# Kernel tuning notes

Measured on AMD Instinct MI355X. Metric: run time of the kernel, lower is better.

Reference implementation:

```python
import jax, jax.numpy as jnp
import numpy as np

SPANS = [15, 9, 5]   # processed largest-first, matching sorted(span_groups, reverse=True)
DEPTH = 2
TOL = 1.5


def _rmsnorm(x, eps=1e-5):
    return x * jax.lax.rsqrt(jnp.mean(x * x, axis=-1, keepdims=True) + eps)


def _block(m, g, Wi, Wz, Wdt, bdt, alog, Wo, Wyg):
    """Dual-input gated selective-scan block (stand-in for create_multihead_block
    block_type='dual_input'): match stream runs a diagonal SSM scan over window
    tokens, gated by the geometry stream; both streams are residually updated."""
    u = _rmsnorm(m) @ Wi                              # [P,L,C]
    z = jax.nn.silu(_rmsnorm(g) @ Wz)                 # [P,L,C] geom gate
    delta = jax.nn.softplus(u @ Wdt + bdt)            # [P,L,C]
    decay = jnp.exp(delta * (-jnp.exp(alog)))         # [P,L,C]
    x_in = delta * u

    def step(h, inp):
        d, xi = inp
        h = d * h + xi
        return h, h

    _, hs = jax.lax.scan(step, jnp.zeros_like(x_in[:, 0]),
                         (jnp.swapaxes(decay, 0, 1), jnp.swapaxes(x_in, 0, 1)))
    y = jnp.swapaxes(hs, 0, 1) * z                    # [P,L,C]
    return m + y @ Wo, g + jax.nn.silu(y @ Wyg)


def _sample(feat_flat, ys, xs, H, W):
    """Bilinear sampling, align_corners=True, padding_mode='zeros'.
    feat_flat: [C, H*W]; ys, xs: [L] float coords. Returns [L, C]."""
    y0 = jnp.floor(ys); x0 = jnp.floor(xs)
    wy = ys - y0; wx = xs - x0

    def tap(yi, xi):
        valid = ((yi >= 0) & (yi <= H - 1) & (xi >= 0) & (xi <= W - 1)).astype(feat_flat.dtype)
        idx = (jnp.clip(yi, 0, H - 1).astype(jnp.int32) * W
               + jnp.clip(xi, 0, W - 1).astype(jnp.int32))
        return feat_flat[:, idx] * valid              # [C,L]

    v = (tap(y0, x0) * (1 - wy) * (1 - wx) + tap(y0, x0 + 1) * (1 - wy) * wx
         + tap(y0 + 1, x0) * wy * (1 - wx) + tap(y0 + 1, x0 + 1) * wy * wx)
    return v.T


def _process_side(feat_m, feat_g, flow, sx, sy, params):
    B, C, H, W = feat_m.shape
    G = feat_g.shape[1]
    Wi, Wz, Wdt, bdt, alog, Wo, Wyg = params
    dt = feat_m.dtype
    bb, yy, xx = [a.ravel() for a in jnp.meshgrid(jnp.arange(B), jnp.arange(H), jnp.arange(W), indexing='ij')]
    # flow-shifted sub-pixel window centers, clamped (flow[...,0]=dx, flow[...,1]=dy)
    cy = jnp.clip(yy.astype(dt) + flow[bb, yy, xx, 1], 0, H - 1)
    cx = jnp.clip(xx.astype(dt) + flow[bb, yy, xx, 0], 0, W - 1)
    avg = ((sx + sy) * 0.5).ravel()
    assigned = jnp.zeros(avg.shape, dtype=bool)
    fm = feat_m.reshape(B, C, H * W)
    fg = feat_g.reshape(B, G, H * W)
    out_m = jnp.zeros((B * H * W, C), dt)
    out_g = jnp.zeros((B * H * W, G), dt)
    wsum = jnp.zeros((B * H * W,), dt)
    for si, s in enumerate(SPANS):
        # span-group mask; positions claimed by a larger span are excluded
        mask = (jnp.abs(avg - s) < TOL) & (~assigned)
        assigned = assigned | mask
        h = s // 2
        dy, dx = [a.ravel() for a in jnp.meshgrid(jnp.arange(-h, h + 1), jnp.arange(-h, h + 1), indexing='ij')]
        dist = jnp.sqrt((dy * dy + dx * dx).astype(dt))
        pw = jnp.exp(-dist / (s / 2.0))
        pw = pw / pw.sum()                             # normalized distance weights [L]
        ys = cy[:, None] + dy[None, :].astype(dt)      # [P,L]
        xs = cx[:, None] + dx[None, :].astype(dt)
        wm = jax.vmap(lambda b, y, x: _sample(fm[b], y, x, H, W))(bb, ys, xs)  # [P,L,C]
        wg = jax.vmap(lambda b, y, x: _sample(fg[b], y, x, H, W))(bb, ys, xs)  # [P,L,G]
        for d in range(DEPTH):
            wm, wg = _block(wm, wg, Wi[si, d], Wz[si, d], Wdt[si, d], bdt[si, d], alog[si, d], Wo[si, d], Wyg[si, d])
        # scatter-accumulate around the integer center position
        ty = yy[:, None] + dy[None, :]
        tx = xx[:, None] + dx[None, :]
        valid = ((ty >= 0) & (ty < H) & (tx >= 0) & (tx < W)).astype(dt)
        w = pw[None, :] * mask[:, None].astype(dt) * valid           # [P,L]
        idx = bb[:, None] * (H * W) + jnp.clip(ty, 0, H - 1) * W + jnp.clip(tx, 0, W - 1)
        out_m = out_m.at[idx.ravel()].add((wm * w[..., None]).reshape(-1, C))
        out_g = out_g.at[idx.ravel()].add((wg * w[..., None]).reshape(-1, G))
        wsum = wsum.at[idx.ravel()].add(w.ravel())
    ws = jnp.maximum(wsum, 1e-6)[:, None]
    om = (out_m / ws).reshape(B, H, W, C).transpose(0, 3, 1, 2)
    og = (out_g / ws).reshape(B, H, W, G).transpose(0, 3, 1, 2)
    return om, og


def setup_inputs() -> dict:
    key = jax.random.key(0)
    ks = jax.random.split(key, 18)
    B, C, G, H, W = 1, 128, 64, 28, 28
    f32 = jnp.float32
    d = {}
    d['feat_match_0'] = jax.random.normal(ks[0], (B, C, H, W), f32)
    d['feat_match_1'] = jax.random.normal(ks[1], (B, C, H, W), f32)
    d['feat_geom_0'] = jax.random.normal(ks[2], (B, G, H, W), f32)
    d['feat_geom_1'] = jax.random.normal(ks[3], (B, G, H, W), f32)
    d['flow_map_0'] = 1.5 * jax.random.normal(ks[4], (B, H, W, 4), f32)
    d['flow_map_1'] = 1.5 * jax.random.normal(ks[5], (B, H, W, 4), f32)
    # spans in [3, 17) so each span group {5, 9, 15} is populated
    d['adaptive_spans_x_0'] = 3.0 + 14.0 * jax.random.uniform(ks[6], (B, H, W), f32)
    d['adaptive_spans_y_0'] = 3.0 + 14.0 * jax.random.uniform(ks[7], (B, H, W), f32)
    d['adaptive_spans_x_1'] = 3.0 + 14.0 * jax.random.uniform(ks[8], (B, H, W), f32)
    d['adaptive_spans_y_1'] = 3.0 + 14.0 * jax.random.uniform(ks[9], (B, H, W), f32)
    # per-span (order [15,9,5]) x per-depth block parameters
    d['W_in'] = jax.random.normal(ks[10], (3, DEPTH, C, C), f32) / np.sqrt(C).astype(np.float32)
    d['W_z'] = jax.random.normal(ks[11], (3, DEPTH, G, C), f32) / np.sqrt(G).astype(np.float32)
    d['W_dt'] = jax.random.normal(ks[12], (3, DEPTH, C, C), f32) / np.sqrt(C).astype(np.float32)
    d['b_dt'] = 0.1 * jax.random.normal(ks[13], (3, DEPTH, C), f32)
    d['a_log'] = 0.1 * jax.random.normal(ks[14], (3, DEPTH, C), f32)
    d['W_out'] = jax.random.normal(ks[15], (3, DEPTH, C, C), f32) / np.sqrt(C).astype(np.float32)
    d['W_yg'] = jax.random.normal(ks[16], (3, DEPTH, C, G), f32) / np.sqrt(C).astype(np.float32)
    return d


def reference(feat_match_0, feat_match_1, feat_geom_0, feat_geom_1,
              flow_map_0, flow_map_1,
              adaptive_spans_x_0, adaptive_spans_y_0,
              adaptive_spans_x_1, adaptive_spans_y_1,
              W_in, W_z, W_dt, b_dt, a_log, W_out, W_yg):
    params = (W_in, W_z, W_dt, b_dt, a_log, W_out, W_yg)
    m0, g0 = _process_side(feat_match_0, feat_geom_0, flow_map_0[..., :2],
                           adaptive_spans_x_0, adaptive_spans_y_0, params)
    m1, g1 = _process_side(feat_match_1, feat_geom_1, flow_map_1[..., :2],
                           adaptive_spans_x_1, adaptive_spans_y_1, params)
    return m0, m1, g0, g1
```

## Files before the change

### kernel.cpp

```cpp
#include <hip/hip_runtime.h>
#include <math.h>

typedef short s16x8 __attribute__((ext_vector_type(8)));
typedef unsigned short u16x8v __attribute__((ext_vector_type(8)));
typedef float f32x4 __attribute__((ext_vector_type(4)));
typedef _Float16 h2 __attribute__((ext_vector_type(2)));

#define HH 28
#define WW 28
#define PP 784
#define CC 128
#define GG 64
#define MT 48
#define NH 3
#define AST 136
#define GSTB 72

#define OFF_FMT0 0
#define OFF_FMT1 100352
#define OFF_FGT0 200704
#define OFF_FGT1 250880
#define OFF_ACCM0 301056
#define OFF_ACCM1 401408
#define OFF_ACCG0 501760
#define OFF_ACCG1 551936
#define OFF_ACCW0 602112
#define OFF_ACCW1 602896
#define ACC_FLOATS 302624
#define OFF_CNT   603680
#define OFF_CNT2  603704
#define OFF_JOB   603728
#define OFF_WB    605296

#define WIB 0
#define WZB 98304
#define WDB 147456
#define WOB 245760
#define WYB 344064

struct KArgs {
  const float* fm[2]; const float* fg[2];
  const float* flow[2]; const float* sx[2]; const float* sy[2];
  const float* Wi; const float* Wz; const float* Wdt; const float* bdt;
  const float* alog; const float* Wo; const float* Wyg;
  float* fmT[2]; float* fgT[2];
  float* accm[2]; float* accg[2]; float* accw[2];
  int* cnt; int* cnt2; int* job;
  unsigned short* wb;
  float* out;
};

__device__ __forceinline__ int span_group(float avg, int& s) {
  if (fabsf(avg - 15.f) < 1.5f) { s = 15; return 0; }
  if (fabsf(avg - 9.f)  < 1.5f) { s = 9;  return 1; }
  if (fabsf(avg - 5.f)  < 1.5f) { s = 5;  return 2; }
  s = 0; return 3;
}

__device__ __forceinline__ float fast_silu(float x) {
  return x * __builtin_amdgcn_rcpf(1.f + __expf(-x));
}

__device__ __forceinline__ unsigned short f2bf(float f) {
  unsigned u = __float_as_uint(f);
  unsigned r = (u + 0x7fffu + ((u >> 16) & 1u)) >> 16;
  return (unsigned short)r;
}
__device__ __forceinline__ float b2f(unsigned short u) {
  return __uint_as_float(((unsigned)u) << 16);
}

__device__ __forceinline__ void atomic_pk2(_Float16* base, float x, float y) {
  h2 v; v[0] = (_Float16)x; v[1] = (_Float16)y;
#if __has_builtin(__builtin_amdgcn_global_atomic_fadd_v2f16)
  __builtin_amdgcn_global_atomic_fadd_v2f16((h2*)base, v);
#else
  unsigned* a = (unsigned*)base;
  unsigned old = *a, assumed;
  do {
    assumed = old;
    h2 cur = *(h2*)&assumed;
    h2 nw; nw[0] = cur[0] + v[0]; nw[1] = cur[1] + v[1];
    old = atomicCAS(a, assumed, *(unsigned*)&nw);
  } while (old != assumed);
#endif
}

#define MFMA(A_, B_, C_) __builtin_amdgcn_mfma_f32_16x16x32_bf16((A_), (B_), (C_), 0, 0, 0)

__global__ void k_zero(float* p, int n) {
  int j = blockIdx.x * 256 + threadIdx.x;
  if (j < n) p[j] = 0.f;
}

__global__ void k_prep(KArgs a) {
  int j = blockIdx.x * 256 + threadIdx.x;
  int side = j / 150528; int r = j - side * 150528;
  int p = r / 192; int ch = r - p * 192;
  if (ch < CC) a.fmT[side][p * CC + ch] = a.fm[side][ch * PP + p];
  else         a.fgT[side][p * GG + (ch - CC)] = a.fg[side][(ch - CC) * PP + p];
}

__global__ void k_prepw(KArgs a) {
  int j = blockIdx.x * 256 + threadIdx.x;
  unsigned short* wb = a.wb;
  if (j < 98304) {
    int set = j >> 14, r = j & 16383; int o = r >> 7, c = r & 127;
    wb[WIB + j] = f2bf(a.Wi[set * 16384 + c * 128 + o]);
  } else if (j < 147456) {
    int r = j - 98304; int set = r >> 13, rr = r & 8191; int o = rr >> 6, c = rr & 63;
    wb[WZB + r] = f2bf(a.Wz[set * 8192 + c * 128 + o]);
  } else if (j < 245760) {
  } else if (j < 344064) {
    int r = j - 245760; int set = r >> 14, rr = r & 16383; int o = rr >> 7, c = rr & 127;
    wb[WOB + r] = f2bf(a.Wo[set * 16384 + c * 128 + o]);
  } else {
    int r = j - 344064; int set = r >> 13, rr = r & 8191; int o = rr >> 7, c = rr & 127;
    wb[WYB + r] = f2bf(a.Wyg[set * 8192 + c * 64 + o]);
  }
}

__global__ void k_prepwid(KArgs a) {
  __shared__ float wi_row[128];
  const int set = blockIdx.x, i = blockIdx.y, o = threadIdx.x;
  wi_row[o] = a.Wi[set * 16384 + i * 128 + o];
  __syncthreads();
  float acc = 0.f;
#pragma unroll 4
  for (int m = 0; m < 128; ++m) acc = fmaf(wi_row[m], a.Wdt[set * 16384 + m * 128 + o], acc);
  a.wb[WDB + set * 16384 + o * 128 + i] = f2bf(acc);
}

__global__ void k_count(KArgs a) {
  int j = blockIdx.x * 256 + threadIdx.x;
  if (j >= 2 * PP) return;
  a.job[j] = -1;
  int side = j / PP, p = j - side * PP;
  float avg = 0.5f * (a.sx[side][p] + a.sy[side][p]);
  int s; int g = span_group(avg, s);
  if (g < 3) {
    int py = p / WW, px = p - py * WW;
    int region = (py / 14) * 4 + px / 7;
    atomicAdd(&a.cnt[region * 3 + g], 1);
  }
}

__global__ void k_assign(KArgs a) {
  int j = blockIdx.x * 256 + threadIdx.x;
  if (j >= 2 * PP) return;
  int side = j / PP, p = j - side * PP;
  float avg = 0.5f * (a.sx[side][p] + a.sy[side][p]);
  int s; int g = span_group(avg, s);
  if (g < 3) {
    int py = p / WW, px = p - py * WW;
    int region = (py / 14) * 4 + px / 7;
    int base = 0;
    for (int gg = 0; gg < g; ++gg) base += a.cnt[region * 3 + gg];
    int rank = base + atomicAdd(&a.cnt2[region * 3 + g], 1);
    a.job[region + 8 * rank] = (side << 10) | p;
  }
}

__global__ void k_fin(KArgs a) {
  int j = blockIdx.x * 256 + threadIdx.x;
  int side = j / 150528; int r = j - side * 150528;
  int p = r / 192; int ch = r - p * 192;
  float inv = 1.f / fmaxf(a.accw[side][p], 1e-6f);
  if (ch < CC) {
    const _Float16* amh = (const _Float16*)a.accm[side];
    a.out[side * 100352 + ch * PP + p] = (float)amh[p * CC + ch] * inv;
  } else {
    const _Float16* agh = (const _Float16*)a.accg[side];
    a.out[200704 + side * 50176 + (ch - CC) * PP + p] = (float)agh[p * GG + (ch - CC)] * inv;
  }
}

__launch_bounds__(256, 2)
__global__ void k_main(KArgs a) {
  __shared__ __align__(16) unsigned short mres[2][MT * AST];
  __shared__ __align__(16) unsigned short gres[2][MT * GSTB];
  __shared__ __align__(16) unsigned short bufA[MT * AST];
  __shared__ __align__(16) unsigned short bufB[MT * GSTB];
  __shared__ float hs[2 * CC];
  __shared__ float na_s[2 * CC];
  __shared__ float bb_s[2 * CC];
  __shared__ float pw_l[228];
  __shared__ int   tap_i[MT * 4];
  __shared__ float tap_w[MT * 4];
  __shared__ int   sc_i[2][MT];
  __shared__ float sc_w[2][MT];
  __shared__ float red[4];

  const int tid = threadIdx.x;
  const int job = a.job[blockIdx.x];
  if (job < 0) return;
  const int side = job >> 10, p = job & 1023;
  const float avg = 0.5f * (a.sx[side][p] + a.sy[side][p]);
  int s; const int si = span_group(avg, s);
  const int hspan = s >> 1, L = s * s;
  const int py = p / WW, px = p - py * WW;
  const float fdx = a.flow[side][p * 4 + 0], fdy = a.flow[side][p * 4 + 1];
  const float cy = fminf(fmaxf((float)py + fdy, 0.f), (float)(HH - 1));
  const float cx = fminf(fmaxf((float)px + fdx, 0.f), (float)(WW - 1));
  const float* fmT = a.fmT[side]; const float* fgT = a.fgT[side];
  _Float16* accm_h = (_Float16*)a.accm[side];
  _Float16* accg_h = (_Float16*)a.accg[side];
  float* accw = a.accw[side];

  const unsigned short* wb = a.wb;
  const int wv = tid >> 6, l = tid & 63, lm = l & 15, g = l >> 4;
  const int o0 = 32 * wv + lm, o1 = o0 + 16, og = 16 * wv + lm;
  const int ttk = tid >> 3, c8 = tid & 7;

  { const int d2 = tid >> 7, c2 = tid & 127;
    na_s[tid] = -__expf(a.alog[(si * 2 + d2) * CC + c2]);
    bb_s[tid] = a.bdt[(si * 2 + d2) * CC + c2];
    hs[tid] = 0.f; }
  if (tid < L) {
    const int dyi = tid / s - hspan, dxi = tid % s - hspan;
    pw_l[tid] = __expf(-sqrtf((float)(dyi * dyi + dxi * dxi)) / (0.5f * (float)s));
  }
  __syncthreads();
  { float v = (tid < L) ? pw_l[tid] : 0.f;
#pragma unroll
    for (int off = 32; off > 0; off >>= 1) v += __shfl_xor(v, off);
    if ((tid & 63) == 0) red[tid >> 6] = v; }
  __syncthreads();
  { const float pinv = 1.f / (red[0] + red[1] + red[2] + red[3]);
    if (tid < L) pw_l[tid] *= pinv; }
  __syncthreads();

  auto comp_taps = [&](int t0_, int b_) {
    if (tid < MT) {
      const int t = t0_ + tid;
      if (t < L) {
        const int tq = t / s;
        const int dyi = tq - hspan, dxi = (t - tq * s) - hspan;
        const float ys = cy + (float)dyi, xs = cx + (float)dxi;
        const float y0f = floorf(ys), x0f = floorf(xs);
        const float wy = ys - y0f, wx = xs - x0f;
        const int y0 = (int)y0f, x0 = (int)x0f;
#pragma unroll
        for (int k = 0; k < 4; ++k) {
          const int yi = y0 + (k >> 1), xi = x0 + (k & 1);
          const bool v = (yi >= 0) && (yi < HH) && (xi >= 0) && (xi < WW);
          const int yc = min(max(yi, 0), HH - 1), xc = min(max(xi, 0), WW - 1);
          tap_i[tid * 4 + k] = yc * WW + xc;
          const float wgt = ((k >> 1) ? wy : 1.f - wy) * ((k & 1) ? wx : 1.f - wx);
          tap_w[tid * 4 + k] = v ? wgt : 0.f;
        }
        const int ty = py + dyi, tx = px + dxi;
        const bool sv = (ty >= 0) && (ty < HH) && (tx >= 0) && (tx < WW);
        const int sid2 = sv ? ty * WW + tx : 0;
        const float sw = sv ? pw_l[t] : 0.f;
        sc_i[b_][tid] = sid2; sc_w[b_][tid] = sw;
        if (sw != 0.f) atomicAdd(&accw[sid2], sw);
      } else {
#pragma unroll
        for (int k = 0; k < 4; ++k) { tap_i[tid * 4 + k] = 0; tap_w[tid * 4 + k] = 0.f; }
        sc_i[b_][tid] = 0; sc_w[b_][tid] = 0.f;
      }
    }
  };

  auto sample_tile = [&](int b_) {
    for (int tk = ttk; tk < MT; tk += 32) {
      const int* ti = &tap_i[tk * 4]; const float* tw = &tap_w[tk * 4];
      f32x4 am0 = {0.f,0.f,0.f,0.f}, am1 = am0, am2 = am0, am3 = am0;
      f32x4 ag0 = am0, ag1 = am0;
#pragma unroll
      for (int k2 = 0; k2 < 4; ++k2) {
        const float w = tw[k2];
        const float* pm = &fmT[ti[k2] * CC + c8 * 16];
        am0 += w * *(const f32x4*)&pm[0];
        am1 += w * *(const f32x4*)&pm[4];
        am2 += w * *(const f32x4*)&pm[8];
        am3 += w * *(const f32x4*)&pm[12];
        const float* pg = &fgT[ti[k2] * GG + c8 * 8];
        ag0 += w * *(const f32x4*)&pg[0];
        ag1 += w * *(const f32x4*)&pg[4];
      }
      u16x8v w0, w1, wg;
#pragma unroll
      for (int j = 0; j < 4; ++j) {
        w0[j] = f2bf(am0[j]); w0[4 + j] = f2bf(am1[j]);
        w1[j] = f2bf(am2[j]); w1[4 + j] = f2bf(am3[j]);
        wg[j] = f2bf(ag0[j]); wg[4 + j] = f2bf(ag1[j]);
      }
      *(u16x8v*)&mres[b_][tk * AST + c8 * 16] = w0;
      *(u16x8v*)&mres[b_][tk * AST + c8 * 16 + 8] = w1;
      *(u16x8v*)&gres[b_][tk * GSTB + c8 * 8] = wg;
    }
  };

  const int nt = (L + MT - 1) / MT;
  comp_taps(0, 0);
  __syncthreads();
  sample_tile(0);
  int cur = 0;

  for (int t = 0; t < nt; ++t) {
    const int t0 = t * MT;
    const int tlen = min(MT, L - t0);
    const int nxt = cur ^ 1;
    __syncthreads();
    if (t + 1 < nt) comp_taps(t0 + MT, nxt);

    for (int d = 0; d < 2; ++d) {
      const unsigned short* Wib  = wb + WIB + (si * 2 + d) * 16384;
      const unsigned short* Widb = wb + WDB + (si * 2 + d) * 16384;
      const unsigned short* Wzb  = wb + WZB + (si * 2 + d) * 8192;
      const unsigned short* Wob  = wb + WOB + (si * 2 + d) * 16384;
      const unsigned short* Wyb  = wb + WYB + (si * 2 + d) * 8192;
      if (d == 1) __syncthreads();
      for (int tk = ttk; tk < MT; tk += 32) {
        u16x8v m0 = *(const u16x8v*)&mres[cur][tk * AST + c8 * 16];
        u16x8v m1 = *(const u16x8v*)&mres[cur][tk * AST + c8 * 16 + 8];
        u16x8v gv = *(const u16x8v*)&gres[cur][tk * GSTB + c8 * 8];
        float mv[16], gvf[8];
#pragma unroll
        for (int k = 0; k < 8; ++k) { mv[k] = b2f(m0[k]); mv[8 + k] = b2f(m1[k]); gvf[k] = b2f(gv[k]); }
        float ssm = 0.f, ssg = 0.f;
#pragma unroll
        for (int k = 0; k < 16; ++k) ssm = fmaf(mv[k], mv[k], ssm);
#pragma unroll
        for (int k = 0; k < 8; ++k) ssg = fmaf(gvf[k], gvf[k], ssg);
#pragma unroll
        for (int off = 4; off > 0; off >>= 1) { ssm += __shfl_xor(ssm, off); ssg += __shfl_xor(ssg, off); }
        const float sm = rsqrtf(ssm * (1.f / CC) + 1e-5f);
        const float sgs = rsqrtf(ssg * (1.f / GG) + 1e-5f);
        u16x8v xa, xb, gx;
#pragma unroll
        for (int k = 0; k < 8; ++k) { xa[k] = f2bf(mv[k] * sm); xb[k] = f2bf(mv[8 + k] * sm); gx[k] = f2bf(gvf[k] * sgs); }
        *(u16x8v*)&bufA[tk * AST + c8 * 16] = xa;
        *(u16x8v*)&bufA[tk * AST + c8 * 16 + 8] = xb;
        *(u16x8v*)&bufB[tk * GSTB + c8 * 8] = gx;
      }
      __syncthreads();
      f32x4 u[NH][2], dt[NH][2], z[NH][2];
#pragma unroll
      for (int h = 0; h < NH; ++h)
#pragma unroll
        for (int j2 = 0; j2 < 2; ++j2) { u[h][j2] = (f32x4){0.f,0.f,0.f,0.f}; dt[h][j2] = (f32x4){0.f,0.f,0.f,0.f}; z[h][j2] = (f32x4){0.f,0.f,0.f,0.f}; }
#pragma unroll
      for (int ss = 0; ss < 4; ++ss) {
        const int c0 = 32 * ss + g * 8;
        const s16x8 bW0 = *(const s16x8*)&Wib[o0 * 128 + c0];
        const s16x8 bW1 = *(const s16x8*)&Wib[o1 * 128 + c0];
        const s16x8 bD0 = *(const s16x8*)&Widb[o0 * 128 + c0];
        const s16x8 bD1 = *(const s16x8*)&Widb[o1 * 128 + c0];
#pragma unroll
        for (int h = 0; h < NH; ++h) {
          s16x8 av = *(const s16x8*)&bufA[(h * 16 + lm) * AST + c0];
          u[h][0]  = MFMA(av, bW0, u[h][0]);
          u[h][1]  = MFMA(av, bW1, u[h][1]);
          dt[h][0] = MFMA(av, bD0, dt[h][0]);
          dt[h][1] = MFMA(av, bD1, dt[h][1]);
        }
      }
#pragma unroll
      for (int ss = 0; ss < 2; ++ss) {
        const int c0 = 32 * ss + g * 8;
        const s16x8 bZ0 = *(const s16x8*)&Wzb[o0 * 64 + c0];
        const s16x8 bZ1 = *(const s16x8*)&Wzb[o1 * 64 + c0];
#pragma unroll
        for (int h = 0; h < NH; ++h) {
          s16x8 gv2 = *(const s16x8*)&bufB[(h * 16 + lm) * GSTB + c0];
          z[h][0] = MFMA(gv2, bZ0, z[h][0]);
          z[h][1] = MFMA(gv2, bZ1, z[h][1]);
        }
      }
#pragma unroll
      for (int h = 0; h < NH; ++h)
#pragma unroll
        for (int j2 = 0; j2 < 2; ++j2)
#pragma unroll
          for (int r = 0; r < 4; ++r) z[h][j2][r] = fast_silu(z[h][j2][r]);

#pragma unroll
      for (int j2 = 0; j2 < 2; ++j2) {
        const int oc = j2 ? o1 : o0;
        const float bb = bb_s[d * CC + oc], na = na_s[d * CC + oc];
        float hcar = hs[d * CC + oc];
#pragma unroll
        for (int h = 0; h < NH; ++h) {
          float Pl[4], Dl[4]; float P = 0.f, D = 1.f;
#pragma unroll
          for (int r = 0; r < 4; ++r) {
            const float x = dt[h][j2][r] + bb;
            float dlt = fmaxf(x, 0.f) + __logf(1.f + __expf(-fabsf(x)));
            float dec = __expf(dlt * na), xin = dlt * u[h][j2][r];
            if (h * 16 + 4 * g + r >= tlen) { dec = 1.f; xin = 0.f; }
            P = dec * P + xin; D *= dec; Pl[r] = P; Dl[r] = D;
          }
          float Pi = P, Di = D;
          { float pa = __shfl_up(Pi, 16), da = __shfl_up(Di, 16);
            if (g >= 1) { Pi = Di * pa + Pi; Di *= da; }
            pa = __shfl_up(Pi, 32); da = __shfl_up(Di, 32);
            if (g >= 2) { Pi = Di * pa + Pi; Di *= da; } }
          float Pe = __shfl_up(Pi, 16), De = __shfl_up(Di, 16);
          if (g == 0) { Pe = 0.f; De = 1.f; }
          const float cr = De * hcar + Pe;
          const float Pf = __shfl(Pi, 48 + lm), Df = __shfl(Di, 48 + lm);
#pragma unroll
          for (int r = 0; r < 4; ++r) z[h][j2][r] = (Dl[r] * cr + Pl[r]) * z[h][j2][r];
          hcar = Df * hcar + Pf;
        }
        if (g == 0) hs[d * CC + oc] = hcar;
      }
      __syncthreads();
#pragma unroll
      for (int h = 0; h < NH; ++h)
#pragma unroll
        for (int r = 0; r < 4; ++r) {
          const int rw = h * 16 + 4 * g + r;
          bufA[rw * AST + o0] = f2bf(z[h][0][r]);
          bufA[rw * AST + o1] = f2bf(z[h][1][r]);
        }
      __syncthreads();
      if (d == 0 && t + 1 < nt) sample_tile(nxt);
      f32x4 dm[NH][2], dgv[NH];
#pragma unroll
      for (int h = 0; h < NH; ++h) { dm[h][0] = (f32x4){0.f,0.f,0.f,0.f}; dm[h][1] = (f32x4){0.f,0.f,0.f,0.f}; dgv[h] = (f32x4){0.f,0.f,0.f,0.f}; }
#pragma unroll
      for (int ss = 0; ss < 4; ++ss) {
        const int c0 = 32 * ss + g * 8;
        const s16x8 bO0 = *(const s16x8*)&Wob[o0 * 128 + c0];
        const s16x8 bO1 = *(const s16x8*)&Wob[o1 * 128 + c0];
        const s16x8 bY  = *(const s16x8*)&Wyb[og * 128 + c0];
#pragma unroll
        for (int h = 0; h < NH; ++h) {
          s16x8 av = *(const s16x8*)&bufA[(h * 16 + lm) * AST + c0];
          dm[h][0] = MFMA(av, bO0, dm[h][0]);
          dm[h][1] = MFMA(av, bO1, dm[h][1]);
          dgv[h]   = MFMA(av, bY, dgv[h]);
        }
      }
      if (d == 0) {
#pragma unroll
        for (int h = 0; h < NH; ++h)
#pragma unroll
          for (int r = 0; r < 4; ++r) {
            const int rw = h * 16 + 4 * g + r;
            mres[cur][rw * AST + o0] = f2bf(b2f(mres[cur][rw * AST + o0]) + dm[h][0][r]);
            mres[cur][rw * AST + o1] = f2bf(b2f(mres[cur][rw * AST + o1]) + dm[h][1][r]);
            gres[cur][rw * GSTB + og] = f2bf(b2f(gres[cur][rw * GSTB + og]) + fast_silu(dgv[h][r]));
          }
      } else {
        const bool evn = (lm & 1) == 0;
#pragma unroll
        for (int h = 0; h < NH; ++h)
#pragma unroll
          for (int r = 0; r < 4; ++r) {
            const int rw = h * 16 + 4 * g + r;
            const float w = sc_w[cur][rw];
            const int tgt = sc_i[cur][rw];
            const float vm0 = (b2f(mres[cur][rw * AST + o0]) + dm[h][0][r]) * w;
            const float vm1 = (b2f(mres[cur][rw * AST + o1]) + dm[h][1][r]) * w;
            const float vg  = (b2f(gres[cur][rw * GSTB + og]) + fast_silu(dgv[h][r])) * w;
            const float pm0 = __shfl_xor(vm0, 1);
            const float pm1 = __shfl_xor(vm1, 1);
            const float pg  = __shfl_xor(vg, 1);
            if (w != 0.f) {
              if (evn) {
                atomic_pk2(accm_h + tgt * CC + o0, vm0, pm0);
                atomic_pk2(accg_h + tgt * GG + og, vg, pg);
              } else {
                atomic_pk2(accm_h + tgt * CC + o1 - 1, pm1, vm1);
              }
            }
          }
      }
    }
    cur = nxt;
  }
}

extern "C" void kernel_launch(void* const* d_in, const int* in_sizes, int n_in,
                              void* d_out, int out_size, void* d_ws, size_t ws_size,
                              hipStream_t stream) {
  (void)in_sizes; (void)n_in; (void)out_size; (void)ws_size;
  float* ws = (float*)d_ws;
  KArgs a;
  a.fm[0]  = (const float*)d_in[0]; a.fm[1]  = (const float*)d_in[1];
  a.fg[0]  = (const float*)d_in[2]; a.fg[1]  = (const float*)d_in[3];
  a.flow[0] = (const float*)d_in[4]; a.flow[1] = (const float*)d_in[5];
  a.sx[0] = (const float*)d_in[6]; a.sy[0] = (const float*)d_in[7];
  a.sx[1] = (const float*)d_in[8]; a.sy[1] = (const float*)d_in[9];
  a.Wi  = (const float*)d_in[10]; a.Wz   = (const float*)d_in[11];
  a.Wdt = (const float*)d_in[12]; a.bdt  = (const float*)d_in[13];
  a.alog = (const float*)d_in[14]; a.Wo  = (const float*)d_in[15];
  a.Wyg = (const float*)d_in[16];
  a.fmT[0] = ws + OFF_FMT0; a.fmT[1] = ws + OFF_FMT1;
  a.fgT[0] = ws + OFF_FGT0; a.fgT[1] = ws + OFF_FGT1;
  a.accm[0] = ws + OFF_ACCM0; a.accm[1] = ws + OFF_ACCM1;
  a.accg[0] = ws + OFF_ACCG0; a.accg[1] = ws + OFF_ACCG1;
  a.accw[0] = ws + OFF_ACCW0; a.accw[1] = ws + OFF_ACCW1;
  a.cnt  = (int*)(ws + OFF_CNT);
  a.cnt2 = (int*)(ws + OFF_CNT2);
  a.job  = (int*)(ws + OFF_JOB);
  a.wb   = (unsigned short*)(ws + OFF_WB);
  a.out = (float*)d_out;

  k_zero<<<1183, 256, 0, stream>>>(ws + OFF_ACCM0, ACC_FLOATS);
  k_zero<<<1, 256, 0, stream>>>(ws + OFF_CNT, 48);
  k_prep<<<1176, 256, 0, stream>>>(a);
  k_prepw<<<1536, 256, 0, stream>>>(a);
  k_prepwid<<<dim3(6, 128), 128, 0, stream>>>(a);
  k_count<<<7, 256, 0, stream>>>(a);
  k_assign<<<7, 256, 0, stream>>>(a);
  k_main<<<1568, 256, 0, stream>>>(a);
  k_fin<<<1176, 256, 0, stream>>>(a);
}
```

Measured before the change: 206.6 us.

## Replace double-buffered LDS sample tiles with register-held gathers to raise occupancy

The next tile's bilinear samples now go into registers (smM/smG) during the depth-0 output phase, instead of into a second LDS buffer for mres/gres. They are written to the single LDS buffer at the start of the next tile. This halves the residual LDS footprint, and launch bounds are raised to 3 blocks per CU to use the freed shared memory. In exchange, each thread holds 12 extra f32x4 registers across the MFMA output phase, which could cause spills or limit occupancy under the tighter register budget.

```diff
diff --git a/kernel.cpp b/kernel.cpp
--- a/kernel.cpp
+++ b/kernel.cpp
@@ -175,10 +175,10 @@
   }
 }
 
-__launch_bounds__(256, 2)
+__launch_bounds__(256, 3)
 __global__ void k_main(KArgs a) {
-  __shared__ __align__(16) unsigned short mres[2][MT * AST];
-  __shared__ __align__(16) unsigned short gres[2][MT * GSTB];
+  __shared__ __align__(16) unsigned short mres[MT * AST];
+  __shared__ __align__(16) unsigned short gres[MT * GSTB];
   __shared__ __align__(16) unsigned short bufA[MT * AST];
   __shared__ __align__(16) unsigned short bufB[MT * GSTB];
   __shared__ float hs[2 * CC];
@@ -263,40 +263,53 @@
     }
   };
 
-  auto sample_tile = [&](int b_) {
-    for (int tk = ttk; tk < MT; tk += 32) {
-      const int* ti = &tap_i[tk * 4]; const float* tw = &tap_w[tk * 4];
-      f32x4 am0 = {0.f,0.f,0.f,0.f}, am1 = am0, am2 = am0, am3 = am0;
-      f32x4 ag0 = am0, ag1 = am0;
-#pragma unroll
-      for (int k2 = 0; k2 < 4; ++k2) {
-        const float w = tw[k2];
-        const float* pm = &fmT[ti[k2] * CC + c8 * 16];
-        am0 += w * *(const f32x4*)&pm[0];
-        am1 += w * *(const f32x4*)&pm[4];
-        am2 += w * *(const f32x4*)&pm[8];
-        am3 += w * *(const f32x4*)&pm[12];
-        const float* pg = &fgT[ti[k2] * GG + c8 * 8];
-        ag0 += w * *(const f32x4*)&pg[0];
-        ag1 += w * *(const f32x4*)&pg[4];
-      }
-      u16x8v w0, w1, wg;
-#pragma unroll
-      for (int j = 0; j < 4; ++j) {
-        w0[j] = f2bf(am0[j]); w0[4 + j] = f2bf(am1[j]);
-        w1[j] = f2bf(am2[j]); w1[4 + j] = f2bf(am3[j]);
-        wg[j] = f2bf(ag0[j]); wg[4 + j] = f2bf(ag1[j]);
-      }
-      *(u16x8v*)&mres[b_][tk * AST + c8 * 16] = w0;
-      *(u16x8v*)&mres[b_][tk * AST + c8 * 16 + 8] = w1;
-      *(u16x8v*)&gres[b_][tk * GSTB + c8 * 8] = wg;
+  f32x4 smM[2][4], smG[2][2];
+  auto gather_tile = [&]() {
+#pragma unroll
+    for (int q = 0; q < 2; ++q) {
+      const int tk = ttk + 32 * q;
+#pragma unroll
+      for (int v = 0; v < 4; ++v) smM[q][v] = (f32x4){0.f,0.f,0.f,0.f};
+#pragma unroll
+      for (int v = 0; v < 2; ++v) smG[q][v] = (f32x4){0.f,0.f,0.f,0.f};
+      if (tk < MT) {
+        const int* ti = &tap_i[tk * 4]; const float* tw = &tap_w[tk * 4];
+#pragma unroll
+        for (int k2 = 0; k2 < 4; ++k2) {
+          const float w = tw[k2];
+          const float* pm = &fmT[ti[k2] * CC + c8 * 16];
+#pragma unroll
+          for (int v = 0; v < 4; ++v) smM[q][v] += w * *(const f32x4*)&pm[4 * v];
+          const float* pg = &fgT[ti[k2] * GG + c8 * 8];
+#pragma unroll
+          for (int v = 0; v < 2; ++v) smG[q][v] += w * *(const f32x4*)&pg[4 * v];
+        }
+      }
+    }
+  };
+  auto write_samples = [&]() {
+#pragma unroll
+    for (int q = 0; q < 2; ++q) {
+      const int tk = ttk + 32 * q;
+      if (tk < MT) {
+        u16x8v w0, w1, wg;
+#pragma unroll
+        for (int j = 0; j < 4; ++j) {
+          w0[j] = f2bf(smM[q][0][j]); w0[4 + j] = f2bf(smM[q][1][j]);
+          w1[j] = f2bf(smM[q][2][j]); w1[4 + j] = f2bf(smM[q][3][j]);
+          wg[j] = f2bf(smG[q][0][j]); wg[4 + j] = f2bf(smG[q][1][j]);
+        }
+        *(u16x8v*)&mres[tk * AST + c8 * 16] = w0;
+        *(u16x8v*)&mres[tk * AST + c8 * 16 + 8] = w1;
+        *(u16x8v*)&gres[tk * GSTB + c8 * 8] = wg;
+      }
     }
   };
 
   const int nt = (L + MT - 1) / MT;
   comp_taps(0, 0);
   __syncthreads();
-  sample_tile(0);
+  gather_tile();
   int cur = 0;
 
   for (int t = 0; t < nt; ++t) {
@@ -304,6 +317,7 @@
     const int tlen = min(MT, L - t0);
     const int nxt = cur ^ 1;
     __syncthreads();
+    write_samples();
     if (t + 1 < nt) comp_taps(t0 + MT, nxt);
 
     for (int d = 0; d < 2; ++d) {
@@ -314,9 +328,9 @@
       const unsigned short* Wyb  = wb + WYB + (si * 2 + d) * 8192;
       if (d == 1) __syncthreads();
       for (int tk = ttk; tk < MT; tk += 32) {
-        u16x8v m0 = *(const u16x8v*)&mres[cur][tk * AST + c8 * 16];
-        u16x8v m1 = *(const u16x8v*)&mres[cur][tk * AST + c8 * 16 + 8];
-        u16x8v gv = *(const u16x8v*)&gres[cur][tk * GSTB + c8 * 8];
+        u16x8v m0 = *(const u16x8v*)&mres[tk * AST + c8 * 16];
+        u16x8v m1 = *(const u16x8v*)&mres[tk * AST + c8 * 16 + 8];
+        u16x8v gv = *(const u16x8v*)&gres[tk * GSTB + c8 * 8];
         float mv[16], gvf[8];
 #pragma unroll
         for (int k = 0; k < 8; ++k) { mv[k] = b2f(m0[k]); mv[8 + k] = b2f(m1[k]); gvf[k] = b2f(gv[k]); }
@@ -418,7 +432,7 @@
           bufA[rw * AST + o1] = f2bf(z[h][1][r]);
         }
       __syncthreads();
-      if (d == 0 && t + 1 < nt) sample_tile(nxt);
+      if (d == 0 && t + 1 < nt) gather_tile();
       f32x4 dm[NH][2], dgv[NH];
 #pragma unroll
       for (int h = 0; h < NH; ++h) { dm[h][0] = (f32x4){0.f,0.f,0.f,0.f}; dm[h][1] = (f32x4){0.f,0.f,0.f,0.f}; dgv[h] = (f32x4){0.f,0.f,0.f,0.f}; }
@@ -442,9 +456,9 @@
 #pragma unroll
           for (int r = 0; r < 4; ++r) {
             const int rw = h * 16 + 4 * g + r;
-            mres[cur][rw * AST + o0] = f2bf(b2f(mres[cur][rw * AST + o0]) + dm[h][0][r]);
-            mres[cur][rw * AST + o1] = f2bf(b2f(mres[cur][rw * AST + o1]) + dm[h][1][r]);
-            gres[cur][rw * GSTB + og] = f2bf(b2f(gres[cur][rw * GSTB + og]) + fast_silu(dgv[h][r]));
+            mres[rw * AST + o0] = f2bf(b2f(mres[rw * AST + o0]) + dm[h][0][r]);
+            mres[rw * AST + o1] = f2bf(b2f(mres[rw * AST + o1]) + dm[h][1][r]);
+            gres[rw * GSTB + og] = f2bf(b2f(gres[rw * GSTB + og]) + fast_silu(dgv[h][r]));
           }
       } else {
         const bool evn = (lm & 1) == 0;
@@ -455,9 +469,9 @@
             const int rw = h * 16 + 4 * g + r;
             const float w = sc_w[cur][rw];
             const int tgt = sc_i[cur][rw];
-            const float vm0 = (b2f(mres[cur][rw * AST + o0]) + dm[h][0][r]) * w;
-            const float vm1 = (b2f(mres[cur][rw * AST + o1]) + dm[h][1][r]) * w;
-            const float vg  = (b2f(gres[cur][rw * GSTB + og]) + fast_silu(dgv[h][r])) * w;
+            const float vm0 = (b2f(mres[rw * AST + o0]) + dm[h][0][r]) * w;
+            const float vm1 = (b2f(mres[rw * AST + o1]) + dm[h][1][r]) * w;
+            const float vg  = (b2f(gres[rw * GSTB + og]) + fast_silu(dgv[h][r])) * w;
             const float pm0 = __shfl_xor(vm0, 1);
             const float pm1 = __shfl_xor(vm1, 1);
             const float pg  = __shfl_xor(vg, 1);
```

Result: slower. 258.1 us (+24.9%).

## Drop double-buffered residual tiles to raise occupancy to three blocks

Applied to the files above, without the earlier changes.

Removes the ping-pong buffers for the match/geometry residual tiles and scatter indices. Sampling of each window tile now happens serially at the top of the loop instead of overlapping the previous tile's block computation. The freed LDS and the launch bound change aim to fit three blocks per CU, hiding latency through occupancy rather than software pipelining. The risks are losing the intra-block overlap, an extra barrier per tile, and tighter register limits.

```diff
diff --git a/kernel.cpp b/kernel.cpp
--- a/kernel.cpp
+++ b/kernel.cpp
@@ -175,10 +175,10 @@
   }
 }
 
-__launch_bounds__(256, 2)
+__launch_bounds__(256, 3)
 __global__ void k_main(KArgs a) {
-  __shared__ __align__(16) unsigned short mres[2][MT * AST];
-  __shared__ __align__(16) unsigned short gres[2][MT * GSTB];
+  __shared__ __align__(16) unsigned short mres[MT * AST];
+  __shared__ __align__(16) unsigned short gres[MT * GSTB];
   __shared__ __align__(16) unsigned short bufA[MT * AST];
   __shared__ __align__(16) unsigned short bufB[MT * GSTB];
   __shared__ float hs[2 * CC];
@@ -187,8 +187,8 @@
   __shared__ float pw_l[228];
   __shared__ int   tap_i[MT * 4];
   __shared__ float tap_w[MT * 4];
-  __shared__ int   sc_i[2][MT];
-  __shared__ float sc_w[2][MT];
+  __shared__ int   sc_i[MT];
+  __shared__ float sc_w[MT];
   __shared__ float red[4];
 
   const int tid = threadIdx.x;
@@ -230,12 +230,16 @@
     if (tid < L) pw_l[tid] *= pinv; }
   __syncthreads();
 
-  auto comp_taps = [&](int t0_, int b_) {
+  const int nt = (L + MT - 1) / MT;
+
+  for (int t = 0; t < nt; ++t) {
+    const int t0 = t * MT;
+    const int tlen = min(MT, L - t0);
     if (tid < MT) {
-      const int t = t0_ + tid;
-      if (t < L) {
-        const int tq = t / s;
-        const int dyi = tq - hspan, dxi = (t - tq * s) - hspan;
+      const int t2 = t0 + tid;
+      if (t2 < L) {
+        const int tq = t2 / s;
+        const int dyi = tq - hspan, dxi = (t2 - tq * s) - hspan;
         const float ys = cy + (float)dyi, xs = cx + (float)dxi;
         const float y0f = floorf(ys), x0f = floorf(xs);
         const float wy = ys - y0f, wx = xs - x0f;
@@ -252,18 +256,16 @@
         const int ty = py + dyi, tx = px + dxi;
         const bool sv = (ty >= 0) && (ty < HH) && (tx >= 0) && (tx < WW);
         const int sid2 = sv ? ty * WW + tx : 0;
-        const float sw = sv ? pw_l[t] : 0.f;
-        sc_i[b_][tid] = sid2; sc_w[b_][tid] = sw;
+        const float sw = sv ? pw_l[t2] : 0.f;
+        sc_i[tid] = sid2; sc_w[tid] = sw;
         if (sw != 0.f) atomicAdd(&accw[sid2], sw);
       } else {
 #pragma unroll
         for (int k = 0; k < 4; ++k) { tap_i[tid * 4 + k] = 0; tap_w[tid * 4 + k] = 0.f; }
-        sc_i[b_][tid] = 0; sc_w[b_][tid] = 0.f;
+        sc_i[tid] = 0; sc_w[tid] = 0.f;
       }
     }
-  };
-
-  auto sample_tile = [&](int b_) {
+    __syncthreads();
     for (int tk = ttk; tk < MT; tk += 32) {
       const int* ti = &tap_i[tk * 4]; const float* tw = &tap_w[tk * 4];
       f32x4 am0 = {0.f,0.f,0.f,0.f}, am1 = am0, am2 = am0, am3 = am0;
@@ -287,24 +289,10 @@
         w1[j] = f2bf(am2[j]); w1[4 + j] = f2bf(am3[j]);
         wg[j] = f2bf(ag0[j]); wg[4 + j] = f2bf(ag1[j]);
       }
-      *(u16x8v*)&mres[b_][tk * AST + c8 * 16] = w0;
-      *(u16x8v*)&mres[b_][tk * AST + c8 * 16 + 8] = w1;
-      *(u16x8v*)&gres[b_][tk * GSTB + c8 * 8] = wg;
+      *(u16x8v*)&mres[tk * AST + c8 * 16] = w0;
+      *(u16x8v*)&mres[tk * AST + c8 * 16 + 8] = w1;
+      *(u16x8v*)&gres[tk * GSTB + c8 * 8] = wg;
     }
-  };
-
-  const int nt = (L + MT - 1) / MT;
-  comp_taps(0, 0);
-  __syncthreads();
-  sample_tile(0);
-  int cur = 0;
-
-  for (int t = 0; t < nt; ++t) {
-    const int t0 = t * MT;
-    const int tlen = min(MT, L - t0);
-    const int nxt = cur ^ 1;
-    __syncthreads();
-    if (t + 1 < nt) comp_taps(t0 + MT, nxt);
 
     for (int d = 0; d < 2; ++d) {
       const unsigned short* Wib  = wb + WIB + (si * 2 + d) * 16384;
@@ -314,9 +302,9 @@
       const unsigned short* Wyb  = wb + WYB + (si * 2 + d) * 8192;
       if (d == 1) __syncthreads();
       for (int tk = ttk; tk < MT; tk += 32) {
-        u16x8v m0 = *(const u16x8v*)&mres[cur][tk * AST + c8 * 16];
-        u16x8v m1 = *(const u16x8v*)&mres[cur][tk * AST + c8 * 16 + 8];
-        u16x8v gv = *(const u16x8v*)&gres[cur][tk * GSTB + c8 * 8];
+        u16x8v m0 = *(const u16x8v*)&mres[tk * AST + c8 * 16];
+        u16x8v m1 = *(const u16x8v*)&mres[tk * AST + c8 * 16 + 8];
+        u16x8v gv = *(const u16x8v*)&gres[tk * GSTB + c8 * 8];
         float mv[16], gvf[8];
 #pragma unroll
         for (int k = 0; k < 8; ++k) { mv[k] = b2f(m0[k]); mv[8 + k] = b2f(m1[k]); gvf[k] = b2f(gv[k]); }
@@ -418,7 +406,6 @@
           bufA[rw * AST + o1] = f2bf(z[h][1][r]);
         }
       __syncthreads();
-      if (d == 0 && t + 1 < nt) sample_tile(nxt);
       f32x4 dm[NH][2], dgv[NH];
 #pragma unroll
       for (int h = 0; h < NH; ++h) { dm[h][0] = (f32x4){0.f,0.f,0.f,0.f}; dm[h][1] = (f32x4){0.f,0.f,0.f,0.f}; dgv[h] = (f32x4){0.f,0.f,0.f,0.f}; }
@@ -442,9 +429,9 @@
 #pragma unroll
           for (int r = 0; r < 4; ++r) {
             const int rw = h * 16 + 4 * g + r;
-            mres[cur][rw * AST + o0] = f2bf(b2f(mres[cur][rw * AST + o0]) + dm[h][0][r]);
-            mres[cur][rw * AST + o1] = f2bf(b2f(mres[cur][rw * AST + o1]) + dm[h][1][r]);
-            gres[cur][rw * GSTB + og] = f2bf(b2f(gres[cur][rw * GSTB + og]) + fast_silu(dgv[h][r]));
+            mres[rw * AST + o0] = f2bf(b2f(mres[rw * AST + o0]) + dm[h][0][r]);
+            mres[rw * AST + o1] = f2bf(b2f(mres[rw * AST + o1]) + dm[h][1][r]);
+            gres[rw * GSTB + og] = f2bf(b2f(gres[rw * GSTB + og]) + fast_silu(dgv[h][r]));
           }
       } else {
         const bool evn = (lm & 1) == 0;
@@ -453,11 +440,11 @@
 #pragma unroll
           for (int r = 0; r < 4; ++r) {
             const int rw = h * 16 + 4 * g + r;
-            const float w = sc_w[cur][rw];
-            const int tgt = sc_i[cur][rw];
-            const float vm0 = (b2f(mres[cur][rw * AST + o0]) + dm[h][0][r]) * w;
-            const float vm1 = (b2f(mres[cur][rw * AST + o1]) + dm[h][1][r]) * w;
-            const float vg  = (b2f(gres[cur][rw * GSTB + og]) + fast_silu(dgv[h][r])) * w;
+            const float w = sc_w[rw];
+            const int tgt = sc_i[rw];
+            const float vm0 = (b2f(mres[rw * AST + o0]) + dm[h][0][r]) * w;
+            const float vm1 = (b2f(mres[rw * AST + o1]) + dm[h][1][r]) * w;
+            const float vg  = (b2f(gres[rw * GSTB + og]) + fast_silu(dgv[h][r])) * w;
             const float pm0 = __shfl_xor(vm0, 1);
             const float pm1 = __shfl_xor(vm1, 1);
             const float pg  = __shfl_xor(vg, 1);
@@ -472,7 +459,7 @@
           }
       }
     }
-    cur = nxt;
+    __syncthreads();
   }
 }
 
```

Measured after the change: 201.2 us (median of 2 runs). 2.6% less time.
